# Kernel tuning notes

Measured on AMD Instinct MI355X. Metric: run time of the kernel, lower is better.

The kernel has to match this reference:

```python
import jax, jax.numpy as jnp
import numpy as np

B, D, DK, DV, NH = 4, 256, 32, 32, 8
HS, WS, RATIO = 64, 64, 2
NQ = HS * WS
EPS_LN = 1e-5
EPS_IN = 1e-5


def setup_inputs() -> dict:
    key = jax.random.key(0)
    ks = jax.random.split(key, 16)
    f = jax.random.normal
    inp = {
        'query': f(ks[0], (B, NQ, D), jnp.float32),
        'key':   f(ks[1], (B, NQ, D), jnp.float32),
        'value': f(ks[2], (B, NQ, D), jnp.float32),
        # Linear weights stored (in, out); torch init std=0.001, bias 0 -- use small std for stability
        'Wq': f(ks[3], (D, DK * NH), jnp.float32) * 0.02,
        'bq': jnp.zeros((DK * NH,), jnp.float32),
        'Wk': f(ks[4], (D, DK * NH), jnp.float32) * 0.02,
        'bk': jnp.zeros((DK * NH,), jnp.float32),
        'Wv': f(ks[5], (D, DV * NH), jnp.float32) * 0.02,
        'bv': jnp.zeros((DV * NH,), jnp.float32),
        'Wo': f(ks[6], (NH * DV, D), jnp.float32) * 0.02,
        'bo': jnp.zeros((D,), jnp.float32),
        # sr_conv: Conv2d(D, D, k=ratio+1=3, stride=2, pad=1), OIHW
        'sr_w': f(ks[7], (D, D, 3, 3), jnp.float32) * (1.0 / np.sqrt(9 * D)),
        'sr_b': jnp.zeros((D,), jnp.float32),
        'ln_g': jnp.ones((D,), jnp.float32),
        'ln_b': jnp.zeros((D,), jnp.float32),
        # transform conv: Conv2d(h, h, 1) -> store as (h, h)
        'tf_w': f(ks[8], (NH, NH), jnp.float32) * (1.0 / np.sqrt(NH)),
        'tf_b': jnp.zeros((NH,), jnp.float32),
    }
    return inp


def _layernorm(x, g, b):
    mu = jnp.mean(x, axis=-1, keepdims=True)
    var = jnp.var(x, axis=-1, keepdims=True)
    return (x - mu) * jax.lax.rsqrt(var + EPS_LN) * g + b


def reference(query, key, value, Wq, bq, Wk, bk, Wv, bv, Wo, bo,
              sr_w, sr_b, ln_g, ln_b, tf_w, tf_b):
    b_s = query.shape[0]
    # q: (b, h, nq, dk)
    q = (query @ Wq + bq).reshape(b_s, NQ, NH, DK).transpose(0, 2, 1, 3)
    # spatial reduction of query: (b, c, H, W) -> conv stride 2 -> (b, c, H/2, W/2)
    x = query.transpose(0, 2, 1).reshape(b_s, D, HS, WS)
    x = jax.lax.conv_general_dilated(
        x, sr_w, window_strides=(RATIO, RATIO), padding=[(1, 1), (1, 1)],
        dimension_numbers=('NCHW', 'OIHW', 'NCHW')) + sr_b[None, :, None, None]
    nk = x.shape[2] * x.shape[3]
    x = x.reshape(b_s, D, nk).transpose(0, 2, 1)  # (b, nk, c)
    x = _layernorm(x, ln_g, ln_b)
    k = (x @ Wk + bk).reshape(b_s, nk, NH, DK).transpose(0, 2, 3, 1)  # (b,h,dk,nk)
    v = (x @ Wv + bv).reshape(b_s, nk, NH, DV).transpose(0, 2, 1, 3)  # (b,h,nk,dv)
    # scores (b,h,nq,nk)
    att = jnp.einsum('bhqd,bhdk->bhqk', q, k) / np.float32(np.sqrt(DK))
    # transform: 1x1 conv mixing heads, softmax over keys, InstanceNorm2d(h) (no affine)
    att = jnp.einsum('oi,biqk->boqk', tf_w, att) + tf_b[None, :, None, None]
    att = jax.nn.softmax(att, axis=-1)
    mu = jnp.mean(att, axis=(2, 3), keepdims=True)
    var = jnp.var(att, axis=(2, 3), keepdims=True)
    att = (att - mu) * jax.lax.rsqrt(var + EPS_IN)
    out = jnp.einsum('bhqk,bhkd->bhqd', att, v)  # (b,h,nq,dv)
    out = out.transpose(0, 2, 1, 3).reshape(b_s, NQ, NH * DV)
    return out @ Wo + bo
```

## Files before the change

kernel.cpp:

```cpp
#include <hip/hip_runtime.h>
#include <hip/hip_bf16.h>
#include <cstdint>


typedef _Float16 f16;
typedef f16 f16x4 __attribute__((ext_vector_type(4)));
typedef f16 f16x8 __attribute__((ext_vector_type(8)));
typedef float f32x4 __attribute__((ext_vector_type(4)));

__launch_bounds__(256)
__global__ void qcvt_zero_kernel(const float* __restrict__ in, f16* __restrict__ out,
                                 float* __restrict__ csum, float* __restrict__ ssq){
    size_t idx = ((size_t)blockIdx.x*256 + threadIdx.x) * 8;
    float4 a = *(const float4*)&in[idx];
    float4 b = *(const float4*)&in[idx+4];
    f16x8 h = { (f16)a.x,(f16)a.y,(f16)a.z,(f16)a.w,(f16)b.x,(f16)b.y,(f16)b.z,(f16)b.w };
    *(f16x8*)&out[idx] = h;
    if (blockIdx.x == 0){
        #pragma unroll
        for (int i = 0; i < 4; ++i) csum[threadIdx.x + i*256] = 0.f;
        if (threadIdx.x < 32) ssq[threadIdx.x] = 0.f;
    }
}

__launch_bounds__(256)
__global__ void wcvtT4_kernel(const float* __restrict__ W0, const float* __restrict__ W1,
                              const float* __restrict__ W2, const float* __restrict__ W3,
                              f16* __restrict__ T0, f16* __restrict__ T1,
                              f16* __restrict__ T2, f16* __restrict__ T3){
    const float* W = (blockIdx.z==0)?W0:(blockIdx.z==1)?W1:(blockIdx.z==2)?W2:W3;
    f16* WT = (blockIdx.z==0)?T0:(blockIdx.z==1)?T1:(blockIdx.z==2)?T2:T3;
    __shared__ float L[32][33];
    int r0 = blockIdx.x*32, c0 = blockIdx.y*32;
    int t = threadIdx.x;
    int rr = t >> 3, cc0 = (t & 7)*4;
    float4 v = *(const float4*)&W[(size_t)(r0+rr)*256 + c0 + cc0];
    L[rr][cc0] = v.x; L[rr][cc0+1] = v.y; L[rr][cc0+2] = v.z; L[rr][cc0+3] = v.w;
    __syncthreads();
    int c = t >> 3, rg = (t & 7)*4;
    f16x4 h = { (f16)L[rg][c], (f16)L[rg+1][c], (f16)L[rg+2][c], (f16)L[rg+3][c] };
    *(f16x4*)&WT[(size_t)(c0+c)*256 + r0 + rg] = h;
}

__launch_bounds__(256)
__global__ void convwT_kernel(const float* __restrict__ w, f16* __restrict__ wtT){
    int o = blockIdx.x, t = threadIdx.x;
    #pragma unroll
    for (int kk = 0; kk < 9; ++kk)
        wtT[(size_t)o*2304 + kk*256 + t] = (f16)w[(size_t)o*2304 + t*9 + kk];
}

template<int BM, int BN, int OUTMODE>
__launch_bounds__(256)
__global__ void mfma_gemm2(const f16* __restrict__ A, const f16* __restrict__ BT,
                           const float* __restrict__ bias, void* __restrict__ Cout,
                           f16* __restrict__ VT, float* __restrict__ csum, int K){
    constexpr int MI = BM/32, NI = BN/32;
    constexpr int AL = BM/64, BL = BN/64;
    __shared__ f16 As[2][BM][40];
    __shared__ f16 Bs[2][BN][40];
    int t = threadIdx.x;
    int wid = t >> 6, l = t & 63;
    int wr = wid >> 1, wc = wid & 1;
    int lr = l & 15, lg = l >> 4;
    int m0 = blockIdx.x * BM, n0 = blockIdx.y * BN;
    int r = t >> 2, c8 = (t & 3)*8;

    f16x8 ra[AL], rb[BL];
    auto loadc = [&](int k0){
        #pragma unroll
        for (int i = 0; i < AL; ++i)
            ra[i] = *(const f16x8*)&A[(size_t)(m0 + r + i*64)*K + k0 + c8];
        #pragma unroll
        for (int i = 0; i < BL; ++i)
            rb[i] = *(const f16x8*)&BT[(size_t)(n0 + r + i*64)*K + k0 + c8];
    };
    auto writec = [&](int b){
        #pragma unroll
        for (int i = 0; i < AL; ++i) *(f16x8*)&As[b][r + i*64][c8] = ra[i];
        #pragma unroll
        for (int i = 0; i < BL; ++i) *(f16x8*)&Bs[b][r + i*64][c8] = rb[i];
    };

    loadc(0); writec(0); loadc(32);
    __syncthreads();

    f32x4 acc[MI][NI] = {};
    const int nsteps = K >> 5;
    for (int s = 0; s < nsteps; ++s){
        int cb = s & 1;
        f16x8 af[MI], bf[NI];
        #pragma unroll
        for (int mi = 0; mi < MI; ++mi)
            af[mi] = *(const f16x8*)&As[cb][wr*(BM/2) + mi*16 + lr][lg*8];
        #pragma unroll
        for (int ni = 0; ni < NI; ++ni)
            bf[ni] = *(const f16x8*)&Bs[cb][wc*(BN/2) + ni*16 + lr][lg*8];
        if (s + 1 < nsteps){
            writec(cb^1);
            if (s + 2 < nsteps) loadc((s+2)*32);
        }
        #pragma unroll
        for (int mi = 0; mi < MI; ++mi)
            #pragma unroll
            for (int ni = 0; ni < NI; ++ni)
                acc[mi][ni] = __builtin_amdgcn_mfma_f32_16x16x32_f16(af[mi], bf[ni], acc[mi][ni], 0, 0, 0);
        if (s + 1 < nsteps) __syncthreads();
    }

    if (OUTMODE == 1){
        #pragma unroll
        for (int mi = 0; mi < MI; ++mi){
            #pragma unroll
            for (int ni = 0; ni < NI; ++ni){
                int n = n0 + wc*(BN/2) + ni*16 + lr;
                float bv = bias[n];
                #pragma unroll
                for (int j = 0; j < 4; ++j){
                    int m = m0 + wr*(BM/2) + mi*16 + lg*4 + j;
                    ((f16*)Cout)[(size_t)m*256 + n] = (f16)(acc[mi][ni][j] + bv);
                }
            }
        }
    } else {
        int b = m0 >> 10;
        #pragma unroll
        for (int ni = 0; ni < NI; ++ni){
            int n = n0 + wc*(BN/2) + ni*16 + lr;
            float bv = bias[n];
            float csp = 0.f;
            #pragma unroll
            for (int mi = 0; mi < MI; ++mi){
                f16x4 hv;
                #pragma unroll
                for (int j = 0; j < 4; ++j){
                    f16 h = (f16)(acc[mi][ni][j] + bv);
                    hv[j] = h;
                    csp += (float)h;
                }
                int m = m0 + wr*(BM/2) + mi*16 + lg*4;
                *(f16x4*)&VT[((size_t)(b*256 + n))*1024 + (m & 1023)] = hv;
            }
            csp += __shfl_xor(csp, 16);
            csp += __shfl_xor(csp, 32);
            if (lg == 0) atomicAdd(&csum[b*256 + n], csp);
        }
    }
}

__launch_bounds__(256)
__global__ void conv2_kernel(const f16* __restrict__ qh, const f16* __restrict__ wtT,
                             const float* __restrict__ srb, float* __restrict__ Xc){
    __shared__ f16 As[2][64][40];
    __shared__ f16 Bs[2][64][40];
    int t = threadIdx.x;
    int wid = t >> 6, l = t & 63;
    int wr = wid >> 1, wc = wid & 1;
    int lr = l & 15, lg = l >> 4;
    int m0 = blockIdx.x * 64, n0 = blockIdx.y * 64;
    int r = t >> 2, c8 = (t & 3)*8;
    int m = m0 + r;
    int bbq = m >> 10, pos = m & 1023;
    int oh = pos >> 5, ow = pos & 31;
    const f16* qb = qh + (size_t)bbq*4096*256;

    f16x8 ra, rbv;
    auto loadc = [&](int k0){
        int khkw = k0 >> 8;
        int kh = (khkw < 3) ? 0 : ((khkw < 6) ? 1 : 2);
        int kw = khkw - kh*3;
        int ih = oh*2 - 1 + kh, iw = ow*2 - 1 + kw;
        int kc = (k0 & 255) + c8;
        f16x8 v = {};
        if ((unsigned)ih < 64u && (unsigned)iw < 64u)
            v = *(const f16x8*)&qb[((size_t)(ih*64 + iw))*256 + kc];
        ra = v;
        rbv = *(const f16x8*)&wtT[(size_t)(n0+r)*2304 + k0 + c8];
    };
    auto writec = [&](int b){
        *(f16x8*)&As[b][r][c8] = ra;
        *(f16x8*)&Bs[b][r][c8] = rbv;
    };

    loadc(0); writec(0); loadc(32);
    __syncthreads();

    f32x4 acc[2][2] = {};
    for (int s = 0; s < 72; ++s){
        int cb = s & 1;
        f16x8 af[2], bf[2];
        #pragma unroll
        for (int mi = 0; mi < 2; ++mi)
            af[mi] = *(const f16x8*)&As[cb][wr*32 + mi*16 + lr][lg*8];
        #pragma unroll
        for (int ni = 0; ni < 2; ++ni)
            bf[ni] = *(const f16x8*)&Bs[cb][wc*32 + ni*16 + lr][lg*8];
        if (s < 71){
            writec(cb^1);
            if (s < 70) loadc((s+2)*32);
        }
        #pragma unroll
        for (int mi = 0; mi < 2; ++mi)
            #pragma unroll
            for (int ni = 0; ni < 2; ++ni)
                acc[mi][ni] = __builtin_amdgcn_mfma_f32_16x16x32_f16(af[mi], bf[ni], acc[mi][ni], 0, 0, 0);
        if (s < 71) __syncthreads();
    }
    #pragma unroll
    for (int mi = 0; mi < 2; ++mi){
        #pragma unroll
        for (int ni = 0; ni < 2; ++ni){
            int n = n0 + wc*32 + ni*16 + lr;
            float bv = srb[n];
            #pragma unroll
            for (int j = 0; j < 4; ++j){
                int mm = m0 + wr*32 + mi*16 + lg*4 + j;
                Xc[(size_t)mm*256 + n] = acc[mi][ni][j] + bv;
            }
        }
    }
}

__launch_bounds__(256)
__global__ void ln_kernel(const float* __restrict__ X, f16* __restrict__ Xo,
                          const float* __restrict__ g, const float* __restrict__ b){
    __shared__ float red[256];
    int row = blockIdx.x, t = threadIdx.x;
    float v = X[(size_t)row*256 + t];
    red[t] = v; __syncthreads();
    #pragma unroll
    for (int s=128; s>0; s>>=1){
        if (t < s) red[t] += red[t+s];
        __syncthreads();
    }
    float mu = red[0] * (1.f/256.f);
    __syncthreads();
    float dv = v - mu;
    red[t] = dv*dv; __syncthreads();
    #pragma unroll
    for (int s=128; s>0; s>>=1){
        if (t < s) red[t] += red[t+s];
        __syncthreads();
    }
    float var = red[0] * (1.f/256.f);
    Xo[(size_t)row*256 + t] = (f16)(dv * rsqrtf(var + 1e-5f) * g[t] + b[t]);
}

__launch_bounds__(512, 4)
__global__ void attn3_kernel(const f16* __restrict__ Qph, const f16* __restrict__ Kh,
                             const f16* __restrict__ VTh, const float* __restrict__ tfw,
                             const float* __restrict__ tfb, const float* __restrict__ csum,
                             float* __restrict__ outu, float* __restrict__ ssq){
    __shared__ f16 KL[2][32][264];
    __shared__ f16 VTL[2][256][40];
    f16 (*QL)[264] = KL[1];

    const int t  = threadIdx.x;
    const int bb = blockIdx.x >> 7;
    const int q0 = (blockIdx.x & 127) * 32;
    const int o  = t >> 6;
    const int l  = t & 63;
    const int g  = l >> 4;
    const int r  = l & 15;

    const f16* Khb = Kh  + (size_t)bb*1024*256;
    const f16* Vtb = VTh + (size_t)bb*256*1024;

    f16x8 rk[2], rv[2];
    #pragma unroll
    for (int it = 0; it < 2; ++it){
        int e = t + it*512;
        int row = e >> 5, c = (e & 31)*8;
        rk[it] = *(const f16x8*)&Khb[(size_t)row*256 + c];
        int d = e >> 2, qt = (e & 3)*8;
        rv[it] = *(const f16x8*)&Vtb[(size_t)d*1024 + qt];
    }
    #pragma unroll
    for (int it = 0; it < 2; ++it){
        int e = t + it*512;
        int row = e >> 5, c = (e & 31)*8;
        f16x8 qv = *(const f16x8*)&Qph[((size_t)(bb*4096 + q0 + row))*256 + c];
        *(f16x8*)&QL[row][c] = qv;
    }
    #pragma unroll
    for (int it = 0; it < 2; ++it){
        int e = t + it*512;
        int row = e >> 5, c = (e & 31)*8;
        *(f16x8*)&KL[0][row][c] = rk[it];
        int d = e >> 2, qt = (e & 3)*8;
        *(f16x8*)&VTL[0][d][qt] = rv[it];
    }
    #pragma unroll
    for (int it = 0; it < 2; ++it){
        int e = t + it*512;
        int row = e >> 5, c = (e & 31)*8;
        rk[it] = *(const f16x8*)&Khb[(size_t)(32 + row)*256 + c];
        int d = e >> 2, qt = (e & 3)*8;
        rv[it] = *(const f16x8*)&Vtb[(size_t)d*1024 + 32 + qt];
    }
    __syncthreads();

    const float LOG2E = 1.4426950408889634f;
    const float tb2 = tfb[o] * LOG2E;
    f16x8 qf[2][8];
    #pragma unroll
    for (int i = 0; i < 8; ++i){
        f16 sc = (f16)(tfw[o*8 + i] * (0.17677669529663687f * LOG2E));
        f16x8 scv = { sc,sc,sc,sc,sc,sc,sc,sc };
        #pragma unroll
        for (int qs = 0; qs < 2; ++qs){
            f16x8 v = *(const f16x8*)&QL[qs*16 + r][i*32 + g*8];
            qf[qs][i] = v * scv;
        }
    }
    __syncthreads();

    f32x4 oacc[2][2] = { { {0,0,0,0},{0,0,0,0} }, { {0,0,0,0},{0,0,0,0} } };
    float s_part[2]  = {0.f, 0.f};
    float q2_part[2] = {0.f, 0.f};

    for (int kci = 0; kci < 32; ++kci){
        const int cb = kci & 1;
        const f16 (*KLc)[264] = KL[cb];
        const f16 (*VTLc)[40] = VTL[cb];

        #pragma unroll
        for (int ks = 0; ks < 2; ++ks){
            f16x4 va0 = *(const f16x4*)&VTLc[o*32 + r][ks*16 + g*4];
            f16x4 va1 = *(const f16x4*)&VTLc[o*32 + 16 + r][ks*16 + g*4];
            f32x4 a0 = {0,0,0,0}, a1 = {0,0,0,0};
            #pragma unroll
            for (int i = 0; i < 8; ++i){
                f16x8 kk = *(const f16x8*)&KLc[ks*16 + r][i*32 + g*8];
                a0 = __builtin_amdgcn_mfma_f32_16x16x32_f16(kk, qf[0][i], a0, 0, 0, 0);
                a1 = __builtin_amdgcn_mfma_f32_16x16x32_f16(kk, qf[1][i], a1, 0, 0, 0);
            }
            #pragma unroll
            for (int qs = 0; qs < 2; ++qs){
                f32x4 aa = qs ? a1 : a0;
                f16x4 pb;
                float ps = 0.f, ps2 = 0.f;
                #pragma unroll
                for (int j = 0; j < 4; ++j){
                    float p = exp2f(aa[j] + tb2);
                    ps += p; ps2 += p*p;
                    pb[j] = (f16)(p - 1.0f);
                }
                s_part[qs]  += ps;
                q2_part[qs] += ps2;
                oacc[qs][0] = __builtin_amdgcn_mfma_f32_16x16x16f16(va0, pb, oacc[qs][0], 0, 0, 0);
                oacc[qs][1] = __builtin_amdgcn_mfma_f32_16x16x16f16(va1, pb, oacc[qs][1], 0, 0, 0);
            }
            if (ks == 0 && kci < 31){
                #pragma unroll
                for (int it = 0; it < 2; ++it){
                    int e = t + it*512;
                    int row = e >> 5, c = (e & 31)*8;
                    *(f16x8*)&KL[cb^1][row][c] = rk[it];
                    int d = e >> 2, qt = (e & 3)*8;
                    *(f16x8*)&VTL[cb^1][d][qt] = rv[it];
                }
                if (kci < 30){
                    int kc2 = (kci + 2) * 32;
                    #pragma unroll
                    for (int it = 0; it < 2; ++it){
                        int e = t + it*512;
                        int row = e >> 5, c = (e & 31)*8;
                        rk[it] = *(const f16x8*)&Khb[(size_t)(kc2 + row)*256 + c];
                        int d = e >> 2, qt = (e & 3)*8;
                        rv[it] = *(const f16x8*)&Vtb[(size_t)d*1024 + kc2 + qt];
                    }
                }
            }
        }
        if (kci < 31) __syncthreads();
    }

    float s2tot = 0.f;
    #pragma unroll
    for (int qs = 0; qs < 2; ++qs){
        float s = s_part[qs];
        s += __shfl_xor(s, 16);
        s += __shfl_xor(s, 32);
        float inv = 1.0f / s;
        float corrf = (1.0f - s * (1.0f/1024.0f)) * inv;
        float q2 = q2_part[qs];
        q2 += __shfl_xor(q2, 16);
        q2 += __shfl_xor(q2, 32);
        s2tot += q2 * inv * inv;
        int q = q0 + qs*16 + r;
        #pragma unroll
        for (int dh = 0; dh < 2; ++dh){
            int d = o*32 + dh*16 + g*4;
            float4 cs = *(const float4*)&csum[bb*256 + d];
            float4 ov;
            ov.x = oacc[qs][dh][0]*inv + cs.x*corrf;
            ov.y = oacc[qs][dh][1]*inv + cs.y*corrf;
            ov.z = oacc[qs][dh][2]*inv + cs.z*corrf;
            ov.w = oacc[qs][dh][3]*inv + cs.w*corrf;
            *(float4*)&outu[((size_t)(bb*4096 + q))*256 + d] = ov;
        }
    }
    s2tot *= 0.25f;
    #pragma unroll
    for (int off = 1; off < 64; off <<= 1)
        s2tot += __shfl_xor(s2tot, off);
    if (l == 0) atomicAdd(&ssq[bb*8 + o], s2tot);
}

__global__ void rs_kernel(const float* __restrict__ ssq, float* __restrict__ rs){
    int t = threadIdx.x;
    const float mu = 1.f/1024.f;
    float var = ssq[t] * (1.f/(4096.f*1024.f)) - mu*mu;
    rs[t] = rsqrtf(var + 1e-5f);
}

__launch_bounds__(256)
__global__ void final2_kernel(const float* __restrict__ A, const f16* __restrict__ WoT,
                              const float* __restrict__ rsb, const float* __restrict__ bo,
                              float* __restrict__ C){
    __shared__ f16 As[2][128][40];
    __shared__ f16 Bs[2][128][40];
    int t = threadIdx.x;
    int wid = t >> 6, l = t & 63;
    int wr = wid >> 1, wc = wid & 1;
    int lr = l & 15, lg = l >> 4;
    int m0 = blockIdx.x * 128, n0 = blockIdx.y * 128;
    int bbatch = m0 >> 12;
    int r = t >> 2, c8 = (t & 3)*8;

    float rs8[8];
    #pragma unroll
    for (int i = 0; i < 8; ++i) rs8[i] = rsb[bbatch*8 + i];

    float4 rfa[4];
    f16x8 rbv[2];
    auto loadc = [&](int k0){
        #pragma unroll
        for (int i = 0; i < 2; ++i){
            const float* ap = &A[(size_t)(m0 + r + i*64)*256 + k0 + c8];
            rfa[2*i]   = *(const float4*)ap;
            rfa[2*i+1] = *(const float4*)(ap+4);
            rbv[i] = *(const f16x8*)&WoT[(size_t)(n0 + r + i*64)*256 + k0 + c8];
        }
    };
    auto writec = [&](int b, int k0){
        float rsk = rs8[k0 >> 5];
        #pragma unroll
        for (int i = 0; i < 2; ++i){
            float4 v0 = rfa[2*i], v1 = rfa[2*i+1];
            f16x8 h = { (f16)(v0.x*rsk),(f16)(v0.y*rsk),(f16)(v0.z*rsk),(f16)(v0.w*rsk),
                        (f16)(v1.x*rsk),(f16)(v1.y*rsk),(f16)(v1.z*rsk),(f16)(v1.w*rsk) };
            *(f16x8*)&As[b][r + i*64][c8] = h;
            *(f16x8*)&Bs[b][r + i*64][c8] = rbv[i];
        }
    };

    loadc(0); writec(0, 0); loadc(32);
    __syncthreads();

    f32x4 acc[4][4] = {};
    for (int s = 0; s < 8; ++s){
        int cb = s & 1;
        f16x8 af[4], bf[4];
        #pragma unroll
        for (int mi = 0; mi < 4; ++mi)
            af[mi] = *(const f16x8*)&As[cb][wr*64 + mi*16 + lr][lg*8];
        #pragma unroll
        for (int ni = 0; ni < 4; ++ni)
            bf[ni] = *(const f16x8*)&Bs[cb][wc*64 + ni*16 + lr][lg*8];
        if (s < 7){
            writec(cb^1, (s+1)*32);
            if (s < 6) loadc((s+2)*32);
        }
        #pragma unroll
        for (int mi = 0; mi < 4; ++mi)
            #pragma unroll
            for (int ni = 0; ni < 4; ++ni)
                acc[mi][ni] = __builtin_amdgcn_mfma_f32_16x16x32_f16(af[mi], bf[ni], acc[mi][ni], 0, 0, 0);
        if (s < 7) __syncthreads();
    }
    #pragma unroll
    for (int mi = 0; mi < 4; ++mi){
        #pragma unroll
        for (int ni = 0; ni < 4; ++ni){
            int n = n0 + wc*64 + ni*16 + lr;
            float bv = bo[n];
            #pragma unroll
            for (int j = 0; j < 4; ++j){
                int m = m0 + wr*64 + mi*16 + lg*4 + j;
                C[(size_t)m*256 + n] = acc[mi][ni][j] + bv;
            }
        }
    }
}

extern "C" void kernel_launch(void* const* d_in, const int* in_sizes, int n_in,
                              void* d_out, int out_size, void* d_ws, size_t ws_size,
                              hipStream_t stream) {
    const float* query = (const float*)d_in[0];
    const float* Wq  = (const float*)d_in[3];
    const float* bq  = (const float*)d_in[4];
    const float* Wk  = (const float*)d_in[5];
    const float* bk  = (const float*)d_in[6];
    const float* Wv  = (const float*)d_in[7];
    const float* bv  = (const float*)d_in[8];
    const float* Wo  = (const float*)d_in[9];
    const float* bo  = (const float*)d_in[10];
    const float* srw = (const float*)d_in[11];
    const float* srb = (const float*)d_in[12];
    const float* lng = (const float*)d_in[13];
    const float* lnb = (const float*)d_in[14];
    const float* tfw = (const float*)d_in[15];
    const float* tfb = (const float*)d_in[16];
    float* out = (float*)d_out;

    float* ws = (float*)d_ws;
    float* outu  = ws;
    f16*   qh    = (f16*)(ws + 4194304);
    f16*   qbh   = (f16*)(ws + 6291456);
    float* xconv = ws + 8388608;
    f16*   xh    = (f16*)(ws + 9437184);
    f16*   kh    = (f16*)(ws + 9961472);
    f16*   vth   = (f16*)(ws + 10485760);
    f16*   wtT   = (f16*)(ws + 11010048);
    f16*   WqT   = (f16*)(ws + 11304960);
    f16*   WkT   = (f16*)(ws + 11337728);
    f16*   WvT   = (f16*)(ws + 11370496);
    f16*   WoT   = (f16*)(ws + 11403264);
    float* csum  = ws + 11436032;
    float* ssq   = ws + 11437056;
    float* rsb   = ws + 11437088;

    qcvt_zero_kernel<<<2048, 256, 0, stream>>>(query, qh, csum, ssq);
    wcvtT4_kernel<<<dim3(8,8,4), 256, 0, stream>>>(Wq, Wk, Wv, Wo, WqT, WkT, WvT, WoT);
    convwT_kernel<<<256, 256, 0, stream>>>(srw, wtT);

    mfma_gemm2<128,128,1><<<dim3(128,2), 256, 0, stream>>>(qh, WqT, bq, qbh, nullptr, nullptr, 256);
    conv2_kernel<<<dim3(64,4), 256, 0, stream>>>(qh, wtT, srb, xconv);
    ln_kernel<<<4096, 256, 0, stream>>>(xconv, xh, lng, lnb);
    mfma_gemm2<64,64,1><<<dim3(64,4), 256, 0, stream>>>(xh, WkT, bk, kh, nullptr, nullptr, 256);
    mfma_gemm2<64,64,2><<<dim3(64,4), 256, 0, stream>>>(xh, WvT, bv, nullptr, vth, csum, 256);
    attn3_kernel<<<512, 512, 0, stream>>>(qbh, kh, vth, tfw, tfb, csum, outu, ssq);
    rs_kernel<<<1, 32, 0, stream>>>(ssq, rsb);
    final2_kernel<<<dim3(128,2), 256, 0, stream>>>(outu, WoT, rsb, bo, out);
}
```

Before: 356.6 us.

## Stream attention K/V tiles straight into LDS with XOR-swizzled layout

The attention kernel now copies K and V^T tiles from global memory straight into LDS using global_load_lds, replacing the old path that staged them through registers. Padded shared arrays are replaced by unpadded buffers addressed with an XOR swizzle, and the Q tile uses the same swizzle. The next chunk's copy is issued at the start of each iteration to overlap with the MFMA work. This frees the staging registers and the ds_write instructions and shrinks LDS use. The cost is more address arithmetic, and correctness now relies on the barrier waiting for the asynchronous LDS writes.

```diff
diff --git a/kernel.cpp b/kernel.cpp
--- a/kernel.cpp
+++ b/kernel.cpp
@@ -7,6 +7,12 @@
 typedef f16 f16x4 __attribute__((ext_vector_type(4)));
 typedef f16 f16x8 __attribute__((ext_vector_type(8)));
 typedef float f32x4 __attribute__((ext_vector_type(4)));
+
+__device__ __forceinline__ void gload16(const void* g, void* l){
+    __builtin_amdgcn_global_load_lds(
+        (const __attribute__((address_space(1))) uint32_t*)g,
+        (__attribute__((address_space(3))) uint32_t*)l, 16, 0, 0);
+}
 
 __launch_bounds__(256)
 __global__ void qcvt_zero_kernel(const float* __restrict__ in, f16* __restrict__ out,
@@ -247,13 +253,12 @@
 }
 
 __launch_bounds__(512, 4)
-__global__ void attn3_kernel(const f16* __restrict__ Qph, const f16* __restrict__ Kh,
+__global__ void attn4_kernel(const f16* __restrict__ Qph, const f16* __restrict__ Kh,
                              const f16* __restrict__ VTh, const float* __restrict__ tfw,
                              const float* __restrict__ tfb, const float* __restrict__ csum,
                              float* __restrict__ outu, float* __restrict__ ssq){
-    __shared__ f16 KL[2][32][264];
-    __shared__ f16 VTL[2][256][40];
-    f16 (*QL)[264] = KL[1];
+    __shared__ f16 KL[2][32*256];
+    __shared__ f16 VTL[2][256*32];
 
     const int t  = threadIdx.x;
     const int bb = blockIdx.x >> 7;
@@ -262,46 +267,44 @@
     const int l  = t & 63;
     const int g  = l >> 4;
     const int r  = l & 15;
-
-    const f16* Khb = Kh  + (size_t)bb*1024*256;
-    const f16* Vtb = VTh + (size_t)bb*256*1024;
-
-    f16x8 rk[2], rv[2];
+    const int wb = o * 2048;
+
+    const char* kbase = (const char*)(Kh  + (size_t)bb*1024*256);
+    const char* vbase = (const char*)(VTh + (size_t)bb*256*1024);
+
+    const int o1 = wb + l*16, o2 = o1 + 1024;
+    const int kr1 = o1 >> 9,  kr2 = o2 >> 9;
+    const char* ks1 = kbase + kr1*512 + ((o1 & 511) ^ ((kr1 & 7) << 4));
+    const char* ks2 = kbase + kr2*512 + ((o2 & 511) ^ ((kr2 & 7) << 4));
+    const int vd1 = o1 >> 6,  vd2 = o2 >> 6;
+    const char* vs1 = vbase + vd1*2048 + ((o1 & 63) ^ ((((vd1&3)^((vd1>>2)&3))) << 4));
+    const char* vs2 = vbase + vd2*2048 + ((o2 & 63) ^ ((((vd2&3)^((vd2>>2)&3))) << 4));
+
+    auto stage = [&](int buf, int chunk){
+        char* kd = (char*)&KL[buf][0]  + wb;
+        char* vd = (char*)&VTL[buf][0] + wb;
+        gload16(ks1 + chunk*16384, kd);
+        gload16(ks2 + chunk*16384, kd + 1024);
+        gload16(vs1 + chunk*64,    vd);
+        gload16(vs2 + chunk*64,    vd + 1024);
+    };
+
+    stage(0, 0);
+
     #pragma unroll
     for (int it = 0; it < 2; ++it){
         int e = t + it*512;
-        int row = e >> 5, c = (e & 31)*8;
-        rk[it] = *(const f16x8*)&Khb[(size_t)row*256 + c];
-        int d = e >> 2, qt = (e & 3)*8;
-        rv[it] = *(const f16x8*)&Vtb[(size_t)d*1024 + qt];
-    }
-    #pragma unroll
-    for (int it = 0; it < 2; ++it){
-        int e = t + it*512;
-        int row = e >> 5, c = (e & 31)*8;
-        f16x8 qv = *(const f16x8*)&Qph[((size_t)(bb*4096 + q0 + row))*256 + c];
-        *(f16x8*)&QL[row][c] = qv;
-    }
-    #pragma unroll
-    for (int it = 0; it < 2; ++it){
-        int e = t + it*512;
-        int row = e >> 5, c = (e & 31)*8;
-        *(f16x8*)&KL[0][row][c] = rk[it];
-        int d = e >> 2, qt = (e & 3)*8;
-        *(f16x8*)&VTL[0][d][qt] = rv[it];
-    }
-    #pragma unroll
-    for (int it = 0; it < 2; ++it){
-        int e = t + it*512;
-        int row = e >> 5, c = (e & 31)*8;
-        rk[it] = *(const f16x8*)&Khb[(size_t)(32 + row)*256 + c];
-        int d = e >> 2, qt = (e & 3)*8;
-        rv[it] = *(const f16x8*)&Vtb[(size_t)d*1024 + 32 + qt];
+        int row = e >> 5;
+        int cb = (e & 31) * 16;
+        f16x8 qv = *(const f16x8*)&Qph[((size_t)(bb*4096 + q0 + row))*256 + (e & 31)*8];
+        *(f16x8*)((char*)&KL[1][0] + row*512 + (cb ^ ((row & 7) << 4))) = qv;
     }
     __syncthreads();
 
     const float LOG2E = 1.4426950408889634f;
     const float tb2 = tfb[o] * LOG2E;
+    const int qsw = (r & 7) << 4;
+    const char* QLb = (const char*)&KL[1][0];
     f16x8 qf[2][8];
     #pragma unroll
     for (int i = 0; i < 8; ++i){
@@ -309,7 +312,7 @@
         f16x8 scv = { sc,sc,sc,sc,sc,sc,sc,sc };
         #pragma unroll
         for (int qs = 0; qs < 2; ++qs){
-            f16x8 v = *(const f16x8*)&QL[qs*16 + r][i*32 + g*8];
+            f16x8 v = *(const f16x8*)(QLb + (qs*16 + r)*512 + ((i*64 + g*16) ^ qsw));
             qf[qs][i] = v * scv;
         }
     }
@@ -318,20 +321,22 @@
     f32x4 oacc[2][2] = { { {0,0,0,0},{0,0,0,0} }, { {0,0,0,0},{0,0,0,0} } };
     float s_part[2]  = {0.f, 0.f};
     float q2_part[2] = {0.f, 0.f};
+    const int vsw = ((r & 3) ^ ((r >> 2) & 3)) << 4;
 
     for (int kci = 0; kci < 32; ++kci){
         const int cb = kci & 1;
-        const f16 (*KLc)[264] = KL[cb];
-        const f16 (*VTLc)[40] = VTL[cb];
+        if (kci < 31) stage(cb^1, kci+1);
+        const char* KLb = (const char*)&KL[cb][0];
+        const char* VLb = (const char*)&VTL[cb][0];
 
         #pragma unroll
         for (int ks = 0; ks < 2; ++ks){
-            f16x4 va0 = *(const f16x4*)&VTLc[o*32 + r][ks*16 + g*4];
-            f16x4 va1 = *(const f16x4*)&VTLc[o*32 + 16 + r][ks*16 + g*4];
+            f16x4 va0 = *(const f16x4*)(VLb + (o*32 + r)*64      + ((ks*32 + g*8) ^ vsw));
+            f16x4 va1 = *(const f16x4*)(VLb + (o*32 + 16 + r)*64 + ((ks*32 + g*8) ^ vsw));
             f32x4 a0 = {0,0,0,0}, a1 = {0,0,0,0};
             #pragma unroll
             for (int i = 0; i < 8; ++i){
-                f16x8 kk = *(const f16x8*)&KLc[ks*16 + r][i*32 + g*8];
+                f16x8 kk = *(const f16x8*)(KLb + (ks*16 + r)*512 + ((i*64 + g*16) ^ qsw));
                 a0 = __builtin_amdgcn_mfma_f32_16x16x32_f16(kk, qf[0][i], a0, 0, 0, 0);
                 a1 = __builtin_amdgcn_mfma_f32_16x16x32_f16(kk, qf[1][i], a1, 0, 0, 0);
             }
@@ -350,27 +355,6 @@
                 q2_part[qs] += ps2;
                 oacc[qs][0] = __builtin_amdgcn_mfma_f32_16x16x16f16(va0, pb, oacc[qs][0], 0, 0, 0);
                 oacc[qs][1] = __builtin_amdgcn_mfma_f32_16x16x16f16(va1, pb, oacc[qs][1], 0, 0, 0);
-            }
-            if (ks == 0 && kci < 31){
-                #pragma unroll
-                for (int it = 0; it < 2; ++it){
-                    int e = t + it*512;
-                    int row = e >> 5, c = (e & 31)*8;
-                    *(f16x8*)&KL[cb^1][row][c] = rk[it];
-                    int d = e >> 2, qt = (e & 3)*8;
-                    *(f16x8*)&VTL[cb^1][d][qt] = rv[it];
-                }
-                if (kci < 30){
-                    int kc2 = (kci + 2) * 32;
-                    #pragma unroll
-                    for (int it = 0; it < 2; ++it){
-                        int e = t + it*512;
-                        int row = e >> 5, c = (e & 31)*8;
-                        rk[it] = *(const f16x8*)&Khb[(size_t)(kc2 + row)*256 + c];
-                        int d = e >> 2, qt = (e & 3)*8;
-                        rv[it] = *(const f16x8*)&Vtb[(size_t)d*1024 + kc2 + qt];
-                    }
-                }
             }
         }
         if (kci < 31) __syncthreads();
@@ -541,7 +525,7 @@
     ln_kernel<<<4096, 256, 0, stream>>>(xconv, xh, lng, lnb);
     mfma_gemm2<64,64,1><<<dim3(64,4), 256, 0, stream>>>(xh, WkT, bk, kh, nullptr, nullptr, 256);
     mfma_gemm2<64,64,2><<<dim3(64,4), 256, 0, stream>>>(xh, WvT, bv, nullptr, vth, csum, 256);
-    attn3_kernel<<<512, 512, 0, stream>>>(qbh, kh, vth, tfw, tfb, csum, outu, ssq);
+    attn4_kernel<<<512, 512, 0, stream>>>(qbh, kh, vth, tfw, tfb, csum, outu, ssq);
     rs_kernel<<<1, 32, 0, stream>>>(ssq, rsb);
     final2_kernel<<<dim3(128,2), 256, 0, stream>>>(outu, WoT, rsb, bo, out);
 }
```

New measurement: 343.0 us. 3.8% less time.
